# Performance work log

Measured on AMD Instinct MI355X. Metric: run time of the kernel, lower is better.

The kernel has to match this reference:

```python
import jax, jax.numpy as jnp
import numpy as np

N = 8            # n_qubits
N_LAYERS_CRZ = 1

_H = jnp.array([[1.0, 1.0], [1.0, -1.0]], dtype=jnp.complex64) / np.sqrt(2).astype(np.float32)
_X2 = jnp.array([[0.0, 1.0], [1.0, 0.0]], dtype=jnp.complex64)
_I2 = jnp.eye(2, dtype=jnp.complex64)


def _apply_1q(state, U, q):
    # shared (2,2) gate on wire q; state: (B, 2,...,2)
    moved = jnp.moveaxis(state, 1 + q, -1)
    out = jnp.einsum('ij,...j->...i', U, moved)
    return jnp.moveaxis(out, -1, 1 + q)


def _apply_1q_batched(state, U, q):
    # per-sample (B,2,2) gate on wire q
    moved = jnp.moveaxis(state, 1 + q, -1)
    out = jnp.einsum('bij,b...j->b...i', U, moved)
    return jnp.moveaxis(out, -1, 1 + q)


def _apply_diag_batched(state, d, q):
    # per-sample diagonal (B,2) phases on wire q
    shape = (d.shape[0],) + (1,) * q + (2,) + (1,) * (N - 1 - q)
    return state * d.reshape(shape)


def _apply_ctrl_diag(state, ph, c, t):
    # controlled diagonal: apply phases ph (2,) on target t when control c == 1
    moved = jnp.moveaxis(state, (1 + c, 1 + t), (-2, -1))
    d = jnp.stack([jnp.ones(2, state.dtype), ph])  # (bc, bt)
    moved = moved * d
    return jnp.moveaxis(moved, (-2, -1), (1 + c, 1 + t))


def _apply_ctrl(state, U, c, t):
    # controlled (2,2) gate, control c, target t
    moved = jnp.moveaxis(state, (1 + c, 1 + t), (-2, -1))
    s0 = moved[..., 0, :]
    s1 = jnp.einsum('ij,...j->...i', U, moved[..., 1, :])
    out = jnp.stack([s0, s1], axis=-2)
    return jnp.moveaxis(out, (-2, -1), (1 + c, 1 + t))


def _circuit(X, weights):
    B = X.shape[0]
    state = jnp.zeros((B,) + (2,) * N, jnp.complex64)
    state = state.at[(slice(None),) + (0,) * N].set(1.0)

    # encoding: H, RZ(x[2q]), RY(x[2q+1]) on each wire q (2q+1 < 16 always)
    for q in range(N):
        state = _apply_1q(state, _H, q)
        th_z = X[:, 2 * q]
        d = jnp.stack([jnp.exp(-0.5j * th_z), jnp.exp(0.5j * th_z)], axis=-1)  # (B,2)
        state = _apply_diag_batched(state, d, q)
        half = 0.5 * X[:, 2 * q + 1]
        c, s = jnp.cos(half), jnp.sin(half)
        Ury = jnp.stack([jnp.stack([c, -s], -1), jnp.stack([s, c], -1)], -2)  # (B,2,2) real
        state = _apply_1q_batched(state, Ury, q)

    # CRZ ring
    for l in range(N_LAYERS_CRZ):
        for i in range(N):
            th = weights[l, i]
            ph = jnp.stack([jnp.exp(-0.5j * th), jnp.exp(0.5j * th)])
            state = _apply_ctrl_diag(state, ph, i, (i + 1) % N)

    # all-to-all CRX
    for i in range(N):
        for j in range(N):
            if j == i:
                continue
            half = 0.5 * weights[N_LAYERS_CRZ + i, j]
            Urx = jnp.cos(half) * _I2 + (-1j * jnp.sin(half)) * _X2
            state = _apply_ctrl(state, Urx, i, j)

    probs = jnp.real(state * jnp.conj(state)).reshape(B, 2 ** N)
    q_idx = jnp.arange(N)
    bits = (jnp.arange(2 ** N)[None, :] >> (N - 1 - q_idx)[:, None]) & 1  # (N, 2^N)
    signs = (1.0 - 2.0 * bits).astype(probs.dtype)
    return probs @ signs.T  # (B, N) <Z_q> expectations


def setup_inputs() -> dict:
    key = jax.random.key(0)
    k1, k2 = jax.random.split(key)
    X = jax.random.normal(k1, (16384, 2 * N), dtype=jnp.float32)
    weights = jax.random.normal(k2, (N_LAYERS_CRZ + N, (N_LAYERS_CRZ + N) * N), dtype=jnp.float32)
    return {"X": X, "weights": weights}


def reference(X, weights):
    return _circuit(X, weights)
```

## Files before the change

kernel.cpp:

```cpp
#include <hip/hip_runtime.h>


static __device__ __forceinline__ float rlane(float v, int src) {
    return __int_as_float(__builtin_amdgcn_readlane(__float_as_int(v), src));
}
template <int CTRL>
static __device__ __forceinline__ float dppf(float x) {
    return __int_as_float(__builtin_amdgcn_update_dpp(0, __float_as_int(x), CTRL, 0xF, 0xF, true));
}
static __device__ __forceinline__ float xor1f(float x) { return dppf<0xB1>(x); }
static __device__ __forceinline__ float xor2f(float x) { return dppf<0x4E>(x); }
static __device__ __forceinline__ float xor4f(float x) { return dppf<0x1B>(dppf<0x141>(x)); }
static __device__ __forceinline__ float xor8f(float x) { return dppf<0x128>(x); }
static __device__ __forceinline__ float xorMf(float x, int m) {
    if (m == 1) return xor1f(x);
    if (m == 2) return xor2f(x);
    if (m == 4) return xor4f(x);
    return xor8f(x);
}
static __device__ __forceinline__ float2 xorM2(float2 a, int m) {
    float2 t; t.x = xorMf(a.x, m); t.y = xorMf(a.y, m); return t;
}
static __device__ __forceinline__ float2 cmul(float2 a, float2 b) {
    float2 t;
    t.x = a.x * b.x - a.y * b.y;
    t.y = a.x * b.y + a.y * b.x;
    return t;
}
static __device__ __forceinline__ float2 rotA(float2 t, float2 u, float c, float s) {
    float2 d;
    d.x = c * t.x + s * u.y;
    d.y = c * t.y - s * u.x;
    return d;
}

__global__ __launch_bounds__(256, 4) void qsim_kernel(const float* __restrict__ X,
                                                      const float* __restrict__ W,
                                                      float* __restrict__ out,
                                                      int B) {
    const int lane = threadIdx.x & 63;
    const int g = lane >> 4;
    const int s = lane & 15;
    const int b = (blockIdx.x * 4 + (threadIdx.x >> 6)) * 4 + g;
    const bool active = (b < B);
    const int bc = active ? b : (B - 1);

    float gcv = 1.0f, gsv = 0.0f;
    if (lane < 56) {
        const int i = lane / 7;
        const int jj = lane - 7 * i;
        const int j = jj + (jj >= i ? 1 : 0);
        const float h = 0.5f * W[(1 + i) * 72 + j];
        __sincosf(h, &gsv, &gcv);
    }

    float u0r, u0i, u1r, u1i;
    {
        const int q = s & 7;
        float2 xq = ((const float2*)X)[bc * 8 + q];
        float cz, sz, cy, sy;
        __sincosf(0.5f * xq.x, &sz, &cz);
        __sincosf(0.5f * xq.y, &sy, &cy);
        u0r = (cy - sy) * cz;  u0i = -(cy + sy) * sz;
        u1r = (cy + sy) * cz;  u1i = (cy - sy) * sz;
    }

    float2 P; P.x = 1.0f; P.y = 0.0f;
#pragma unroll
    for (int q = 4; q < 8; ++q) {
        const int src = (g << 4) + q;
        const float a0r = __shfl(u0r, src, 64), a0i = __shfl(u0i, src, 64);
        const float a1r = __shfl(u1r, src, 64), a1i = __shfl(u1i, src, 64);
        const int bit = (s >> (7 - q)) & 1;
        float2 v; v.x = bit ? a1r : a0r; v.y = bit ? a1i : a0i;
        P = cmul(P, v);
    }
    float2 w0[4], w1[4];
#pragma unroll
    for (int k = 0; k < 4; ++k) {
        const int src = (g << 4) + k;
        w0[k].x = __shfl(u0r, src, 64);  w0[k].y = __shfl(u0i, src, 64);
        w1[k].x = __shfl(u1r, src, 64);  w1[k].y = __shfl(u1i, src, 64);
    }
    float2 a[16];
    {
        float2 t1[2];
        t1[0] = w0[0];
        t1[1] = w1[0];
        float2 t2[4];
#pragma unroll
        for (int h = 0; h < 2; ++h) {
            t2[h * 2 + 0] = cmul(t1[h], w0[1]);
            t2[h * 2 + 1] = cmul(t1[h], w1[1]);
        }
        float2 t3[8];
#pragma unroll
        for (int h = 0; h < 4; ++h) {
            t3[h * 2 + 0] = cmul(t2[h], w0[2]);
            t3[h * 2 + 1] = cmul(t2[h], w1[2]);
        }
#pragma unroll
        for (int h = 0; h < 8; ++h) {
            a[h * 2 + 0] = cmul(P, cmul(t3[h], w0[3]));
            a[h * 2 + 1] = cmul(P, cmul(t3[h], w1[3]));
        }
    }

    {
        const float wv0 = W[0], wv1 = W[1], wv2 = W[2], wv3 = W[3];
        const float wv4 = W[4], wv5 = W[5], wv6 = W[6], wv7 = W[7];
        const int s3 = (s >> 3) & 1, s2 = (s >> 2) & 1, s1 = (s >> 1) & 1, s0 = s & 1;
        float phiS = 0.0f;
        phiS += s3 ? (s2 ? wv4 : -wv4) : 0.0f;
        phiS += s2 ? (s1 ? wv5 : -wv5) : 0.0f;
        phiS += s1 ? (s0 ? wv6 : -wv6) : 0.0f;
        const float termA = s3 ? wv3 : -wv3;
        const float termB = s0 ? wv7 : 0.0f;
#pragma unroll
        for (int r = 0; r < 16; ++r) {
            const int b3 = (r >> 3) & 1, b2 = (r >> 2) & 1, b1 = (r >> 1) & 1, b0 = r & 1;
            float phi = phiS + (b3 ? termB : -termB);
            if (b3) phi += b2 ? wv0 : -wv0;
            if (b2) phi += b1 ? wv1 : -wv1;
            if (b1) phi += b0 ? wv2 : -wv2;
            if (b0) phi += termA;
            float2 ph;
            __sincosf(0.5f * phi, &ph.y, &ph.x);
            a[r] = cmul(a[r], ph);
        }
    }

#pragma unroll
    for (int i = 0; i < 4; ++i) {
        float cg[8], sg[8];
#pragma unroll
        for (int j = 0; j < 8; ++j) {
            if (j == i) continue;
            const int gi = i * 7 + (j < i ? j : j - 1);
            cg[j] = rlane(gcv, gi);
            sg[j] = rlane(gsv, gi);
        }
        const int rc = 3 - i;
#pragma unroll
        for (int j = 0; j < 8; ++j) {
            if (j == i) continue;
            if (j < 4) {
                const int mt = 1 << (3 - j);
#pragma unroll
                for (int r = 0; r < 16; ++r) {
                    if (!((r >> rc) & 1)) continue;
                    if (r & mt) continue;
                    const int rp = r | mt;
                    const float2 t = a[r], u = a[rp];
                    a[r]  = rotA(t, u, cg[j], sg[j]);
                    a[rp] = rotA(u, t, cg[j], sg[j]);
                }
            } else {
                const int ms = 1 << (7 - j);
#pragma unroll
                for (int r = 0; r < 16; ++r) {
                    if (!((r >> rc) & 1)) continue;
                    const float2 p = xorM2(a[r], ms);
                    a[r] = rotA(a[r], p, cg[j], sg[j]);
                }
            }
        }
    }

#pragma unroll
    for (int k = 1; k <= 8; k <<= 1) {
        const bool sk = (s & k) != 0;
#pragma unroll
        for (int r = 0; r < 16; ++r) {
            if (r & k) continue;
            const int rp = r | k;
            const float2 tp = xorM2(a[rp], k);
            const float2 tr = xorM2(a[r],  k);
            a[r].x  = sk ? tp.x : a[r].x;
            a[r].y  = sk ? tp.y : a[r].y;
            a[rp].x = sk ? a[rp].x : tr.x;
            a[rp].y = sk ? a[rp].y : tr.y;
        }
    }

#pragma unroll
    for (int i = 4; i < 8; ++i) {
        float cg[8], sg[8];
#pragma unroll
        for (int j = 0; j < 8; ++j) {
            if (j == i) continue;
            const int gi = i * 7 + (j < i ? j : j - 1);
            cg[j] = rlane(gcv, gi);
            sg[j] = rlane(gsv, gi);
        }
        const int rc = 7 - i;
#pragma unroll
        for (int j = 0; j < 8; ++j) {
            if (j == i) continue;
            if (j < 4) {
                const int ms = 1 << (3 - j);
#pragma unroll
                for (int r = 0; r < 16; ++r) {
                    if (!((r >> rc) & 1)) continue;
                    const float2 p = xorM2(a[r], ms);
                    a[r] = rotA(a[r], p, cg[j], sg[j]);
                }
            } else {
                const int mt = 1 << (7 - j);
#pragma unroll
                for (int r = 0; r < 16; ++r) {
                    if (!((r >> rc) & 1)) continue;
                    if (r & mt) continue;
                    const int rp = r | mt;
                    const float2 t = a[r], u = a[rp];
                    a[r]  = rotA(t, u, cg[j], sg[j]);
                    a[rp] = rotA(u, t, cg[j], sg[j]);
                }
            }
        }
    }

    float p[16];
#pragma unroll
    for (int r = 0; r < 16; ++r) p[r] = a[r].x * a[r].x + a[r].y * a[r].y;
    float s8[8], E7 = 0.0f;
#pragma unroll
    for (int k = 0; k < 8; ++k) { s8[k] = p[2 * k] + p[2 * k + 1]; E7 += p[2 * k] - p[2 * k + 1]; }
    float s4[4], E6 = 0.0f;
#pragma unroll
    for (int k = 0; k < 4; ++k) { s4[k] = s8[2 * k] + s8[2 * k + 1]; E6 += s8[2 * k] - s8[2 * k + 1]; }
    float s2a[2], E5 = 0.0f;
#pragma unroll
    for (int k = 0; k < 2; ++k) { s2a[k] = s4[2 * k] + s4[2 * k + 1]; E5 += s4[2 * k] - s4[2 * k + 1]; }
    float A  = s2a[0] + s2a[1];
    float E4 = s2a[0] - s2a[1];
    float D0, D1, D2, D3;
    { const float t = xor1f(A); D0 = A - t; A += t;
      E4 += xor1f(E4); E5 += xor1f(E5); E6 += xor1f(E6); E7 += xor1f(E7); }
    { const float t = xor2f(A); D1 = A - t; A += t;
      D0 += xor2f(D0);
      E4 += xor2f(E4); E5 += xor2f(E5); E6 += xor2f(E6); E7 += xor2f(E7); }
    { const float t = xor4f(A); D2 = A - t; A += t;
      D0 += xor4f(D0); D1 += xor4f(D1);
      E4 += xor4f(E4); E5 += xor4f(E5); E6 += xor4f(E6); E7 += xor4f(E7); }
    { const float t = xor8f(A); D3 = A - t;
      D0 += xor8f(D0); D1 += xor8f(D1); D2 += xor8f(D2);
      E4 += xor8f(E4); E5 += xor8f(E5); E6 += xor8f(E6); E7 += xor8f(E7); }

    if (s == 0 && active) {
        const float sc = 1.0f / 256.0f;
        float* o = out + b * 8;
        o[0] = D3 * sc;
        o[1] = D2 * sc;
        o[2] = D1 * sc;
        o[3] = D0 * sc;
        o[4] = E4 * sc;
        o[5] = E5 * sc;
        o[6] = E6 * sc;
        o[7] = E7 * sc;
    }
}

extern "C" void kernel_launch(void* const* d_in, const int* in_sizes, int n_in,
                              void* d_out, int out_size, void* d_ws, size_t ws_size,
                              hipStream_t stream) {
    const float* X = (const float*)d_in[0];
    const float* W = (const float*)d_in[1];
    float* out = (float*)d_out;
    const int B = in_sizes[0] / 16;
    const int blocks = (B + 15) / 16;
    qsim_kernel<<<blocks, 256, 0, stream>>>(X, W, out, B);
}
```

Measured before the change: 76.86 us.

## Spread each sample's state over 32 lanes with 8 amplitudes per lane

Changes the state distribution from 16 lanes × 16 amplitudes to 32 lanes × 8 amplitudes per sample, so each wave handles two samples instead of four. The mid-circuit transpose between qubit halves is removed: gates controlled by lane-resident qubits are applied uniformly with a per-lane select of cos/sin. Cross-lane exchanges use DPP plus a ds_swizzle for the xor-16 partner. The aim is to cut register pressure (launch bounds raised to 8 waves per SIMD) and drop the shuffle-heavy transpose, at the cost of more cross-lane traffic and redundant rotations on lanes where the control bit is zero.

```diff
diff --git a/kernel.cpp b/kernel.cpp
--- a/kernel.cpp
+++ b/kernel.cpp
@@ -8,15 +8,19 @@
 static __device__ __forceinline__ float dppf(float x) {
     return __int_as_float(__builtin_amdgcn_update_dpp(0, __float_as_int(x), CTRL, 0xF, 0xF, true));
 }
-static __device__ __forceinline__ float xor1f(float x) { return dppf<0xB1>(x); }
-static __device__ __forceinline__ float xor2f(float x) { return dppf<0x4E>(x); }
-static __device__ __forceinline__ float xor4f(float x) { return dppf<0x1B>(dppf<0x141>(x)); }
-static __device__ __forceinline__ float xor8f(float x) { return dppf<0x128>(x); }
+static __device__ __forceinline__ float xor1f(float x)  { return dppf<0xB1>(x); }
+static __device__ __forceinline__ float xor2f(float x)  { return dppf<0x4E>(x); }
+static __device__ __forceinline__ float xor4f(float x)  { return dppf<0x1B>(dppf<0x141>(x)); }
+static __device__ __forceinline__ float xor8f(float x)  { return dppf<0x128>(x); }
+static __device__ __forceinline__ float xor16f(float x) {
+    return __int_as_float(__builtin_amdgcn_ds_swizzle(__float_as_int(x), 0x401F));
+}
 static __device__ __forceinline__ float xorMf(float x, int m) {
-    if (m == 1) return xor1f(x);
-    if (m == 2) return xor2f(x);
-    if (m == 4) return xor4f(x);
-    return xor8f(x);
+    if (m == 1)  return xor1f(x);
+    if (m == 2)  return xor2f(x);
+    if (m == 4)  return xor4f(x);
+    if (m == 8)  return xor8f(x);
+    return xor16f(x);
 }
 static __device__ __forceinline__ float2 xorM2(float2 a, int m) {
     float2 t; t.x = xorMf(a.x, m); t.y = xorMf(a.y, m); return t;
@@ -34,14 +38,14 @@
     return d;
 }
 
-__global__ __launch_bounds__(256, 4) void qsim_kernel(const float* __restrict__ X,
+__global__ __launch_bounds__(256, 8) void qsim_kernel(const float* __restrict__ X,
                                                       const float* __restrict__ W,
                                                       float* __restrict__ out,
                                                       int B) {
     const int lane = threadIdx.x & 63;
-    const int g = lane >> 4;
-    const int s = lane & 15;
-    const int b = (blockIdx.x * 4 + (threadIdx.x >> 6)) * 4 + g;
+    const int e  = lane >> 5;
+    const int s5 = lane & 31;
+    const int b = (blockIdx.x * 4 + (threadIdx.x >> 6)) * 2 + e;
     const bool active = (b < B);
     const int bc = active ? b : (B - 1);
 
@@ -56,7 +60,7 @@
 
     float u0r, u0i, u1r, u1i;
     {
-        const int q = s & 7;
+        const int q = s5 & 7;
         float2 xq = ((const float2*)X)[bc * 8 + q];
         float cz, sz, cy, sy;
         __sincosf(0.5f * xq.x, &sz, &cz);
@@ -67,22 +71,22 @@
 
     float2 P; P.x = 1.0f; P.y = 0.0f;
 #pragma unroll
-    for (int q = 4; q < 8; ++q) {
-        const int src = (g << 4) + q;
+    for (int q = 0; q < 5; ++q) {
+        const int src = (e << 5) + q;
         const float a0r = __shfl(u0r, src, 64), a0i = __shfl(u0i, src, 64);
         const float a1r = __shfl(u1r, src, 64), a1i = __shfl(u1i, src, 64);
-        const int bit = (s >> (7 - q)) & 1;
+        const int bit = (s5 >> (4 - q)) & 1;
         float2 v; v.x = bit ? a1r : a0r; v.y = bit ? a1i : a0i;
         P = cmul(P, v);
     }
-    float2 w0[4], w1[4];
-#pragma unroll
-    for (int k = 0; k < 4; ++k) {
-        const int src = (g << 4) + k;
+    float2 w0[3], w1[3];
+#pragma unroll
+    for (int k = 0; k < 3; ++k) {
+        const int src = (e << 5) + 5 + k;
         w0[k].x = __shfl(u0r, src, 64);  w0[k].y = __shfl(u0i, src, 64);
         w1[k].x = __shfl(u1r, src, 64);  w1[k].y = __shfl(u1i, src, 64);
     }
-    float2 a[16];
+    float2 a[8];
     {
         float2 t1[2];
         t1[0] = w0[0];
@@ -93,37 +97,32 @@
             t2[h * 2 + 0] = cmul(t1[h], w0[1]);
             t2[h * 2 + 1] = cmul(t1[h], w1[1]);
         }
-        float2 t3[8];
 #pragma unroll
         for (int h = 0; h < 4; ++h) {
-            t3[h * 2 + 0] = cmul(t2[h], w0[2]);
-            t3[h * 2 + 1] = cmul(t2[h], w1[2]);
-        }
-#pragma unroll
-        for (int h = 0; h < 8; ++h) {
-            a[h * 2 + 0] = cmul(P, cmul(t3[h], w0[3]));
-            a[h * 2 + 1] = cmul(P, cmul(t3[h], w1[3]));
+            a[h * 2 + 0] = cmul(P, cmul(t2[h], w0[2]));
+            a[h * 2 + 1] = cmul(P, cmul(t2[h], w1[2]));
         }
     }
 
     {
         const float wv0 = W[0], wv1 = W[1], wv2 = W[2], wv3 = W[3];
         const float wv4 = W[4], wv5 = W[5], wv6 = W[6], wv7 = W[7];
-        const int s3 = (s >> 3) & 1, s2 = (s >> 2) & 1, s1 = (s >> 1) & 1, s0 = s & 1;
+        const int s4b = (s5 >> 4) & 1, s3b = (s5 >> 3) & 1, s2b = (s5 >> 2) & 1;
+        const int s1b = (s5 >> 1) & 1, s0b = s5 & 1;
         float phiS = 0.0f;
-        phiS += s3 ? (s2 ? wv4 : -wv4) : 0.0f;
-        phiS += s2 ? (s1 ? wv5 : -wv5) : 0.0f;
-        phiS += s1 ? (s0 ? wv6 : -wv6) : 0.0f;
-        const float termA = s3 ? wv3 : -wv3;
-        const float termB = s0 ? wv7 : 0.0f;
-#pragma unroll
-        for (int r = 0; r < 16; ++r) {
-            const int b3 = (r >> 3) & 1, b2 = (r >> 2) & 1, b1 = (r >> 1) & 1, b0 = r & 1;
-            float phi = phiS + (b3 ? termB : -termB);
-            if (b3) phi += b2 ? wv0 : -wv0;
-            if (b2) phi += b1 ? wv1 : -wv1;
-            if (b1) phi += b0 ? wv2 : -wv2;
-            if (b0) phi += termA;
+        phiS += s4b ? (s3b ? wv0 : -wv0) : 0.0f;
+        phiS += s3b ? (s2b ? wv1 : -wv1) : 0.0f;
+        phiS += s2b ? (s1b ? wv2 : -wv2) : 0.0f;
+        phiS += s1b ? (s0b ? wv3 : -wv3) : 0.0f;
+        const float termA = s0b ? wv4 : 0.0f;
+        const float termB = s4b ? wv7 : -wv7;
+#pragma unroll
+        for (int r = 0; r < 8; ++r) {
+            const int b2 = (r >> 2) & 1, b1 = (r >> 1) & 1, b0 = r & 1;
+            float phi = phiS + (b2 ? termA : -termA);
+            if (b2) phi += b1 ? wv5 : -wv5;
+            if (b1) phi += b0 ? wv6 : -wv6;
+            if (b0) phi += termB;
             float2 ph;
             __sincosf(0.5f * phi, &ph.y, &ph.x);
             a[r] = cmul(a[r], ph);
@@ -131,7 +130,7 @@
     }
 
 #pragma unroll
-    for (int i = 0; i < 4; ++i) {
+    for (int i = 0; i < 8; ++i) {
         float cg[8], sg[8];
 #pragma unroll
         for (int j = 0; j < 8; ++j) {
@@ -140,121 +139,96 @@
             cg[j] = rlane(gcv, gi);
             sg[j] = rlane(gsv, gi);
         }
-        const int rc = 3 - i;
-#pragma unroll
-        for (int j = 0; j < 8; ++j) {
-            if (j == i) continue;
-            if (j < 4) {
-                const int mt = 1 << (3 - j);
-#pragma unroll
-                for (int r = 0; r < 16; ++r) {
-                    if (!((r >> rc) & 1)) continue;
-                    if (r & mt) continue;
-                    const int rp = r | mt;
-                    const float2 t = a[r], u = a[rp];
-                    a[r]  = rotA(t, u, cg[j], sg[j]);
-                    a[rp] = rotA(u, t, cg[j], sg[j]);
-                }
-            } else {
-                const int ms = 1 << (7 - j);
-#pragma unroll
-                for (int r = 0; r < 16; ++r) {
-                    if (!((r >> rc) & 1)) continue;
-                    const float2 p = xorM2(a[r], ms);
-                    a[r] = rotA(a[r], p, cg[j], sg[j]);
+        if (i <= 4) {
+            const int cbit = (s5 >> (4 - i)) & 1;
+#pragma unroll
+            for (int j = 0; j < 8; ++j) {
+                if (j == i) continue;
+                const float ce = cbit ? cg[j] : 1.0f;
+                const float se = cbit ? sg[j] : 0.0f;
+                if (j <= 4) {
+                    const int ms = 1 << (4 - j);
+#pragma unroll
+                    for (int r = 0; r < 8; ++r) {
+                        const float2 p = xorM2(a[r], ms);
+                        a[r] = rotA(a[r], p, ce, se);
+                    }
+                } else {
+                    const int mt = 1 << (7 - j);
+#pragma unroll
+                    for (int r = 0; r < 8; ++r) {
+                        if (r & mt) continue;
+                        const int rp = r | mt;
+                        const float2 t = a[r], u = a[rp];
+                        a[r]  = rotA(t, u, ce, se);
+                        a[rp] = rotA(u, t, ce, se);
+                    }
                 }
             }
-        }
-    }
-
-#pragma unroll
-    for (int k = 1; k <= 8; k <<= 1) {
-        const bool sk = (s & k) != 0;
-#pragma unroll
-        for (int r = 0; r < 16; ++r) {
-            if (r & k) continue;
-            const int rp = r | k;
-            const float2 tp = xorM2(a[rp], k);
-            const float2 tr = xorM2(a[r],  k);
-            a[r].x  = sk ? tp.x : a[r].x;
-            a[r].y  = sk ? tp.y : a[r].y;
-            a[rp].x = sk ? a[rp].x : tr.x;
-            a[rp].y = sk ? a[rp].y : tr.y;
-        }
-    }
-
-#pragma unroll
-    for (int i = 4; i < 8; ++i) {
-        float cg[8], sg[8];
-#pragma unroll
-        for (int j = 0; j < 8; ++j) {
-            if (j == i) continue;
-            const int gi = i * 7 + (j < i ? j : j - 1);
-            cg[j] = rlane(gcv, gi);
-            sg[j] = rlane(gsv, gi);
-        }
-        const int rc = 7 - i;
-#pragma unroll
-        for (int j = 0; j < 8; ++j) {
-            if (j == i) continue;
-            if (j < 4) {
-                const int ms = 1 << (3 - j);
-#pragma unroll
-                for (int r = 0; r < 16; ++r) {
-                    if (!((r >> rc) & 1)) continue;
-                    const float2 p = xorM2(a[r], ms);
-                    a[r] = rotA(a[r], p, cg[j], sg[j]);
-                }
-            } else {
-                const int mt = 1 << (7 - j);
-#pragma unroll
-                for (int r = 0; r < 16; ++r) {
-                    if (!((r >> rc) & 1)) continue;
-                    if (r & mt) continue;
-                    const int rp = r | mt;
-                    const float2 t = a[r], u = a[rp];
-                    a[r]  = rotA(t, u, cg[j], sg[j]);
-                    a[rp] = rotA(u, t, cg[j], sg[j]);
+        } else {
+            const int rc = 7 - i;
+#pragma unroll
+            for (int j = 0; j < 8; ++j) {
+                if (j == i) continue;
+                if (j <= 4) {
+                    const int ms = 1 << (4 - j);
+#pragma unroll
+                    for (int r = 0; r < 8; ++r) {
+                        if (!((r >> rc) & 1)) continue;
+                        const float2 p = xorM2(a[r], ms);
+                        a[r] = rotA(a[r], p, cg[j], sg[j]);
+                    }
+                } else {
+                    const int mt = 1 << (7 - j);
+#pragma unroll
+                    for (int r = 0; r < 8; ++r) {
+                        if (!((r >> rc) & 1)) continue;
+                        if (r & mt) continue;
+                        const int rp = r | mt;
+                        const float2 t = a[r], u = a[rp];
+                        a[r]  = rotA(t, u, cg[j], sg[j]);
+                        a[rp] = rotA(u, t, cg[j], sg[j]);
+                    }
                 }
             }
         }
     }
 
-    float p[16];
-#pragma unroll
-    for (int r = 0; r < 16; ++r) p[r] = a[r].x * a[r].x + a[r].y * a[r].y;
-    float s8[8], E7 = 0.0f;
-#pragma unroll
-    for (int k = 0; k < 8; ++k) { s8[k] = p[2 * k] + p[2 * k + 1]; E7 += p[2 * k] - p[2 * k + 1]; }
-    float s4[4], E6 = 0.0f;
-#pragma unroll
-    for (int k = 0; k < 4; ++k) { s4[k] = s8[2 * k] + s8[2 * k + 1]; E6 += s8[2 * k] - s8[2 * k + 1]; }
-    float s2a[2], E5 = 0.0f;
-#pragma unroll
-    for (int k = 0; k < 2; ++k) { s2a[k] = s4[2 * k] + s4[2 * k + 1]; E5 += s4[2 * k] - s4[2 * k + 1]; }
-    float A  = s2a[0] + s2a[1];
-    float E4 = s2a[0] - s2a[1];
-    float D0, D1, D2, D3;
-    { const float t = xor1f(A); D0 = A - t; A += t;
-      E4 += xor1f(E4); E5 += xor1f(E5); E6 += xor1f(E6); E7 += xor1f(E7); }
-    { const float t = xor2f(A); D1 = A - t; A += t;
+    float p[8];
+#pragma unroll
+    for (int r = 0; r < 8; ++r) p[r] = a[r].x * a[r].x + a[r].y * a[r].y;
+    float s4v[4], E7 = 0.0f;
+#pragma unroll
+    for (int k = 0; k < 4; ++k) { s4v[k] = p[2 * k] + p[2 * k + 1]; E7 += p[2 * k] - p[2 * k + 1]; }
+    float s2v[2], E6 = 0.0f;
+#pragma unroll
+    for (int k = 0; k < 2; ++k) { s2v[k] = s4v[2 * k] + s4v[2 * k + 1]; E6 += s4v[2 * k] - s4v[2 * k + 1]; }
+    float A  = s2v[0] + s2v[1];
+    float E5 = s2v[0] - s2v[1];
+    float D0, D1, D2, D3, D4;
+    { const float t = xor1f(A);  D0 = A - t; A += t;
+      E5 += xor1f(E5);  E6 += xor1f(E6);  E7 += xor1f(E7); }
+    { const float t = xor2f(A);  D1 = A - t; A += t;
       D0 += xor2f(D0);
-      E4 += xor2f(E4); E5 += xor2f(E5); E6 += xor2f(E6); E7 += xor2f(E7); }
-    { const float t = xor4f(A); D2 = A - t; A += t;
-      D0 += xor4f(D0); D1 += xor4f(D1);
-      E4 += xor4f(E4); E5 += xor4f(E5); E6 += xor4f(E6); E7 += xor4f(E7); }
-    { const float t = xor8f(A); D3 = A - t;
-      D0 += xor8f(D0); D1 += xor8f(D1); D2 += xor8f(D2);
-      E4 += xor8f(E4); E5 += xor8f(E5); E6 += xor8f(E6); E7 += xor8f(E7); }
-
-    if (s == 0 && active) {
+      E5 += xor2f(E5);  E6 += xor2f(E6);  E7 += xor2f(E7); }
+    { const float t = xor4f(A);  D2 = A - t; A += t;
+      D0 += xor4f(D0);  D1 += xor4f(D1);
+      E5 += xor4f(E5);  E6 += xor4f(E6);  E7 += xor4f(E7); }
+    { const float t = xor8f(A);  D3 = A - t; A += t;
+      D0 += xor8f(D0);  D1 += xor8f(D1);  D2 += xor8f(D2);
+      E5 += xor8f(E5);  E6 += xor8f(E6);  E7 += xor8f(E7); }
+    { const float t = xor16f(A); D4 = A - t;
+      D0 += xor16f(D0); D1 += xor16f(D1); D2 += xor16f(D2); D3 += xor16f(D3);
+      E5 += xor16f(E5); E6 += xor16f(E6); E7 += xor16f(E7); }
+
+    if (s5 == 0 && active) {
         const float sc = 1.0f / 256.0f;
         float* o = out + b * 8;
-        o[0] = D3 * sc;
-        o[1] = D2 * sc;
-        o[2] = D1 * sc;
-        o[3] = D0 * sc;
-        o[4] = E4 * sc;
+        o[0] = D4 * sc;
+        o[1] = D3 * sc;
+        o[2] = D2 * sc;
+        o[3] = D1 * sc;
+        o[4] = D0 * sc;
         o[5] = E5 * sc;
         o[6] = E6 * sc;
         o[7] = E7 * sc;
@@ -268,6 +242,6 @@
     const float* W = (const float*)d_in[1];
     float* out = (float*)d_out;
     const int B = in_sizes[0] / 16;
-    const int blocks = (B + 15) / 16;
+    const int blocks = (B + 7) / 8;
     qsim_kernel<<<blocks, 256, 0, stream>>>(X, W, out, B);
 }
```

After: 84.73 us. 10.3% more time.

## Roll CRX control loops with register bit-rotation to shrink code size

Applied to the files above, without the earlier changes.

The fully unrolled CRX loops over control qubits are replaced by non-unrolled loops (unroll 1). Each iteration always treats the upper half of the register array as the control=1 subset, then rotates the register bit indices so the next control qubit lands in the top bit. DPP cross-lane values are gathered into temporaries before the rotations are applied, which may improve instruction scheduling. The aim is smaller instruction footprint and lower register pressure, at the cost of loop overhead and register permutation moves that the compiler must resolve as copies.

```diff
diff --git a/kernel.cpp b/kernel.cpp
--- a/kernel.cpp
+++ b/kernel.cpp
@@ -17,9 +17,6 @@
     if (m == 2) return xor2f(x);
     if (m == 4) return xor4f(x);
     return xor8f(x);
-}
-static __device__ __forceinline__ float2 xorM2(float2 a, int m) {
-    float2 t; t.x = xorMf(a.x, m); t.y = xorMf(a.y, m); return t;
 }
 static __device__ __forceinline__ float2 cmul(float2 a, float2 b) {
     float2 t;
@@ -130,41 +127,44 @@
         }
     }
 
-#pragma unroll
-    for (int i = 0; i < 4; ++i) {
-        float cg[8], sg[8];
-#pragma unroll
-        for (int j = 0; j < 8; ++j) {
-            if (j == i) continue;
-            const int gi = i * 7 + (j < i ? j : j - 1);
-            cg[j] = rlane(gcv, gi);
-            sg[j] = rlane(gsv, gi);
-        }
-        const int rc = 3 - i;
-#pragma unroll
-        for (int j = 0; j < 8; ++j) {
-            if (j == i) continue;
-            if (j < 4) {
-                const int mt = 1 << (3 - j);
-#pragma unroll
-                for (int r = 0; r < 16; ++r) {
-                    if (!((r >> rc) & 1)) continue;
-                    if (r & mt) continue;
-                    const int rp = r | mt;
-                    const float2 t = a[r], u = a[rp];
-                    a[r]  = rotA(t, u, cg[j], sg[j]);
-                    a[rp] = rotA(u, t, cg[j], sg[j]);
-                }
-            } else {
-                const int ms = 1 << (7 - j);
-#pragma unroll
-                for (int r = 0; r < 16; ++r) {
-                    if (!((r >> rc) & 1)) continue;
-                    const float2 p = xorM2(a[r], ms);
-                    a[r] = rotA(a[r], p, cg[j], sg[j]);
-                }
-            }
-        }
+#pragma unroll 1
+    for (int it = 0; it < 4; ++it) {
+#pragma unroll
+        for (int tp = 2; tp >= 0; --tp) {
+            const int p = (tp - it) & 3;
+            const int j = 3 - p;
+            const int gi = it * 7 + (j < it ? j : j - 1);
+            const float c  = rlane(gcv, gi);
+            const float sn = rlane(gsv, gi);
+            const int mt = 1 << tp;
+#pragma unroll
+            for (int r = 8; r < 16; ++r) {
+                if (r & mt) continue;
+                const int rp = r | mt;
+                const float2 t = a[r], u = a[rp];
+                a[r]  = rotA(t, u, c, sn);
+                a[rp] = rotA(u, t, c, sn);
+            }
+        }
+#pragma unroll
+        for (int j = 4; j < 8; ++j) {
+            const int gi = it * 7 + (j - 1);
+            const float c  = rlane(gcv, gi);
+            const float sn = rlane(gsv, gi);
+            const int ms = 1 << (7 - j);
+            float pr[8], pi[8];
+#pragma unroll
+            for (int r = 8; r < 16; ++r) { pr[r - 8] = xorMf(a[r].x, ms); pi[r - 8] = xorMf(a[r].y, ms); }
+#pragma unroll
+            for (int r = 8; r < 16; ++r) {
+                float2 pp; pp.x = pr[r - 8]; pp.y = pi[r - 8];
+                a[r] = rotA(a[r], pp, c, sn);
+            }
+        }
+        { float2 t = a[8];  a[8]  = a[4];  a[4]  = a[2];  a[2]  = a[1];  a[1]  = t; }
+        { float2 t = a[9];  a[9]  = a[12]; a[12] = a[6];  a[6]  = a[3];  a[3]  = t; }
+        { float2 t = a[5];  a[5]  = a[10]; a[10] = t; }
+        { float2 t = a[11]; a[11] = a[13]; a[13] = a[14]; a[14] = a[7];  a[7]  = t; }
     }
 
 #pragma unroll
@@ -174,50 +174,55 @@
         for (int r = 0; r < 16; ++r) {
             if (r & k) continue;
             const int rp = r | k;
-            const float2 tp = xorM2(a[rp], k);
-            const float2 tr = xorM2(a[r],  k);
-            a[r].x  = sk ? tp.x : a[r].x;
-            a[r].y  = sk ? tp.y : a[r].y;
-            a[rp].x = sk ? a[rp].x : tr.x;
-            a[rp].y = sk ? a[rp].y : tr.y;
-        }
-    }
-
-#pragma unroll
-    for (int i = 4; i < 8; ++i) {
-        float cg[8], sg[8];
-#pragma unroll
-        for (int j = 0; j < 8; ++j) {
-            if (j == i) continue;
+            float2 tp2, tr2;
+            tp2.x = xorMf(a[rp].x, k); tp2.y = xorMf(a[rp].y, k);
+            tr2.x = xorMf(a[r].x,  k); tr2.y = xorMf(a[r].y,  k);
+            a[r].x  = sk ? tp2.x : a[r].x;
+            a[r].y  = sk ? tp2.y : a[r].y;
+            a[rp].x = sk ? a[rp].x : tr2.x;
+            a[rp].y = sk ? a[rp].y : tr2.y;
+        }
+    }
+
+#pragma unroll 1
+    for (int it = 0; it < 4; ++it) {
+        const int i = it + 4;
+#pragma unroll
+        for (int j = 0; j < 4; ++j) {
+            const int gi = i * 7 + j;
+            const float c  = rlane(gcv, gi);
+            const float sn = rlane(gsv, gi);
+            const int ms = 1 << (3 - j);
+            float pr[8], pi[8];
+#pragma unroll
+            for (int r = 8; r < 16; ++r) { pr[r - 8] = xorMf(a[r].x, ms); pi[r - 8] = xorMf(a[r].y, ms); }
+#pragma unroll
+            for (int r = 8; r < 16; ++r) {
+                float2 pp; pp.x = pr[r - 8]; pp.y = pi[r - 8];
+                a[r] = rotA(a[r], pp, c, sn);
+            }
+        }
+#pragma unroll
+        for (int tp = 2; tp >= 0; --tp) {
+            const int p = (tp - it) & 3;
+            const int j = 7 - p;
             const int gi = i * 7 + (j < i ? j : j - 1);
-            cg[j] = rlane(gcv, gi);
-            sg[j] = rlane(gsv, gi);
-        }
-        const int rc = 7 - i;
-#pragma unroll
-        for (int j = 0; j < 8; ++j) {
-            if (j == i) continue;
-            if (j < 4) {
-                const int ms = 1 << (3 - j);
-#pragma unroll
-                for (int r = 0; r < 16; ++r) {
-                    if (!((r >> rc) & 1)) continue;
-                    const float2 p = xorM2(a[r], ms);
-                    a[r] = rotA(a[r], p, cg[j], sg[j]);
-                }
-            } else {
-                const int mt = 1 << (7 - j);
-#pragma unroll
-                for (int r = 0; r < 16; ++r) {
-                    if (!((r >> rc) & 1)) continue;
-                    if (r & mt) continue;
-                    const int rp = r | mt;
-                    const float2 t = a[r], u = a[rp];
-                    a[r]  = rotA(t, u, cg[j], sg[j]);
-                    a[rp] = rotA(u, t, cg[j], sg[j]);
-                }
-            }
-        }
+            const float c  = rlane(gcv, gi);
+            const float sn = rlane(gsv, gi);
+            const int mt = 1 << tp;
+#pragma unroll
+            for (int r = 8; r < 16; ++r) {
+                if (r & mt) continue;
+                const int rp = r | mt;
+                const float2 t = a[r], u = a[rp];
+                a[r]  = rotA(t, u, c, sn);
+                a[rp] = rotA(u, t, c, sn);
+            }
+        }
+        { float2 t = a[8];  a[8]  = a[4];  a[4]  = a[2];  a[2]  = a[1];  a[1]  = t; }
+        { float2 t = a[9];  a[9]  = a[12]; a[12] = a[6];  a[6]  = a[3];  a[3]  = t; }
+        { float2 t = a[5];  a[5]  = a[10]; a[10] = t; }
+        { float2 t = a[11]; a[11] = a[13]; a[13] = a[14]; a[14] = a[7];  a[7]  = t; }
     }
 
     float p[16];
```

Measured after the change: 80.67 us. 1.05x slower.

## Precompute fixed entangling unitary and apply it via fp16 MFMA GEMM

Applied to the files above, without the earlier changes.

Splits the kernel in two. The first kernel builds the 256x256 unitary of the weight-only CRZ/CRX section by pushing basis vectors through the old gate code, and stores it as fp16 real and imaginary parts in the workspace. The second kernel builds each sample's product-state vector in LDS and multiplies it by that unitary with 16x16x32 f16 MFMA instructions, then reduces the probabilities to Z expectations. This replaces per-sample gate-by-gate simulation with a dense complex GEMM, at the cost of fp16 rounding error and an extra kernel launch.

```diff
diff --git a/kernel.cpp b/kernel.cpp
--- a/kernel.cpp
+++ b/kernel.cpp
@@ -1,5 +1,9 @@
 #include <hip/hip_runtime.h>
 
+
+typedef _Float16 half_t;
+typedef __attribute__((ext_vector_type(8))) _Float16 half8;
+typedef __attribute__((ext_vector_type(4))) float float4v;
 
 static __device__ __forceinline__ float rlane(float v, int src) {
     return __int_as_float(__builtin_amdgcn_readlane(__float_as_int(v), src));
@@ -34,16 +38,13 @@
     return d;
 }
 
-__global__ __launch_bounds__(256, 4) void qsim_kernel(const float* __restrict__ X,
-                                                      const float* __restrict__ W,
-                                                      float* __restrict__ out,
-                                                      int B) {
+__global__ __launch_bounds__(256, 4) void buildV_kernel(const float* __restrict__ W,
+                                                        half_t* __restrict__ Vr,
+                                                        half_t* __restrict__ Vi) {
     const int lane = threadIdx.x & 63;
     const int g = lane >> 4;
     const int s = lane & 15;
-    const int b = (blockIdx.x * 4 + (threadIdx.x >> 6)) * 4 + g;
-    const bool active = (b < B);
-    const int bc = active ? b : (B - 1);
+    const int eid = (blockIdx.x * 4 + (threadIdx.x >> 6)) * 4 + g;
 
     float gcv = 1.0f, gsv = 0.0f;
     if (lane < 56) {
@@ -54,56 +55,11 @@
         __sincosf(h, &gsv, &gcv);
     }
 
-    float u0r, u0i, u1r, u1i;
-    {
-        const int q = s & 7;
-        float2 xq = ((const float2*)X)[bc * 8 + q];
-        float cz, sz, cy, sy;
-        __sincosf(0.5f * xq.x, &sz, &cz);
-        __sincosf(0.5f * xq.y, &sy, &cy);
-        u0r = (cy - sy) * cz;  u0i = -(cy + sy) * sz;
-        u1r = (cy + sy) * cz;  u1i = (cy - sy) * sz;
-    }
-
-    float2 P; P.x = 1.0f; P.y = 0.0f;
-#pragma unroll
-    for (int q = 4; q < 8; ++q) {
-        const int src = (g << 4) + q;
-        const float a0r = __shfl(u0r, src, 64), a0i = __shfl(u0i, src, 64);
-        const float a1r = __shfl(u1r, src, 64), a1i = __shfl(u1i, src, 64);
-        const int bit = (s >> (7 - q)) & 1;
-        float2 v; v.x = bit ? a1r : a0r; v.y = bit ? a1i : a0i;
-        P = cmul(P, v);
-    }
-    float2 w0[4], w1[4];
-#pragma unroll
-    for (int k = 0; k < 4; ++k) {
-        const int src = (g << 4) + k;
-        w0[k].x = __shfl(u0r, src, 64);  w0[k].y = __shfl(u0i, src, 64);
-        w1[k].x = __shfl(u1r, src, 64);  w1[k].y = __shfl(u1i, src, 64);
-    }
     float2 a[16];
-    {
-        float2 t1[2];
-        t1[0] = w0[0];
-        t1[1] = w1[0];
-        float2 t2[4];
-#pragma unroll
-        for (int h = 0; h < 2; ++h) {
-            t2[h * 2 + 0] = cmul(t1[h], w0[1]);
-            t2[h * 2 + 1] = cmul(t1[h], w1[1]);
-        }
-        float2 t3[8];
-#pragma unroll
-        for (int h = 0; h < 4; ++h) {
-            t3[h * 2 + 0] = cmul(t2[h], w0[2]);
-            t3[h * 2 + 1] = cmul(t2[h], w1[2]);
-        }
-#pragma unroll
-        for (int h = 0; h < 8; ++h) {
-            a[h * 2 + 0] = cmul(P, cmul(t3[h], w0[3]));
-            a[h * 2 + 1] = cmul(P, cmul(t3[h], w1[3]));
-        }
+#pragma unroll
+    for (int r = 0; r < 16; ++r) {
+        a[r].x = (s == (eid & 15) && r == (eid >> 4)) ? 1.0f : 0.0f;
+        a[r].y = 0.0f;
     }
 
     {
@@ -220,44 +176,164 @@
         }
     }
 
-    float p[16];
-#pragma unroll
-    for (int r = 0; r < 16; ++r) p[r] = a[r].x * a[r].x + a[r].y * a[r].y;
-    float s8[8], E7 = 0.0f;
-#pragma unroll
-    for (int k = 0; k < 8; ++k) { s8[k] = p[2 * k] + p[2 * k + 1]; E7 += p[2 * k] - p[2 * k + 1]; }
-    float s4[4], E6 = 0.0f;
-#pragma unroll
-    for (int k = 0; k < 4; ++k) { s4[k] = s8[2 * k] + s8[2 * k + 1]; E6 += s8[2 * k] - s8[2 * k + 1]; }
-    float s2a[2], E5 = 0.0f;
-#pragma unroll
-    for (int k = 0; k < 2; ++k) { s2a[k] = s4[2 * k] + s4[2 * k + 1]; E5 += s4[2 * k] - s4[2 * k + 1]; }
-    float A  = s2a[0] + s2a[1];
-    float E4 = s2a[0] - s2a[1];
-    float D0, D1, D2, D3;
-    { const float t = xor1f(A); D0 = A - t; A += t;
-      E4 += xor1f(E4); E5 += xor1f(E5); E6 += xor1f(E6); E7 += xor1f(E7); }
-    { const float t = xor2f(A); D1 = A - t; A += t;
-      D0 += xor2f(D0);
-      E4 += xor2f(E4); E5 += xor2f(E5); E6 += xor2f(E6); E7 += xor2f(E7); }
-    { const float t = xor4f(A); D2 = A - t; A += t;
-      D0 += xor4f(D0); D1 += xor4f(D1);
-      E4 += xor4f(E4); E5 += xor4f(E5); E6 += xor4f(E6); E7 += xor4f(E7); }
-    { const float t = xor8f(A); D3 = A - t;
-      D0 += xor8f(D0); D1 += xor8f(D1); D2 += xor8f(D2);
-      E4 += xor8f(E4); E5 += xor8f(E5); E6 += xor8f(E6); E7 += xor8f(E7); }
-
-    if (s == 0 && active) {
-        const float sc = 1.0f / 256.0f;
-        float* o = out + b * 8;
-        o[0] = D3 * sc;
-        o[1] = D2 * sc;
-        o[2] = D1 * sc;
-        o[3] = D0 * sc;
-        o[4] = E4 * sc;
-        o[5] = E5 * sc;
-        o[6] = E6 * sc;
-        o[7] = E7 * sc;
+    const int ks = eid >> 5, kq = (eid >> 3) & 3, jj = eid & 7;
+#pragma unroll
+    for (int r = 0; r < 16; ++r) {
+        const int off = ((s * 8 + ks) * 64 + kq * 16 + r) * 8 + jj;
+        Vr[off] = (half_t)a[r].x;
+        Vi[off] = (half_t)a[r].y;
+    }
+}
+
+#define PSI_STRIDE 264
+
+__global__ __launch_bounds__(256, 2) void gemm_kernel(const float* __restrict__ X,
+                                                      const half_t* __restrict__ Vr,
+                                                      const half_t* __restrict__ Vi,
+                                                      float* __restrict__ out,
+                                                      int B) {
+    __shared__ float4 u_lds[32][8];
+    __shared__ half_t psir[32][PSI_STRIDE];
+    __shared__ half_t psii[32][PSI_STRIDE];
+    __shared__ float part[32][8][4];
+
+    const int tid = threadIdx.x;
+    const int rowbase = blockIdx.x * 32;
+
+    {
+        const int m = tid >> 3, q = tid & 7;
+        int row = rowbase + m; if (row >= B) row = B - 1;
+        const float2 xq = ((const float2*)X)[row * 8 + q];
+        float cz, sz, cy, sy;
+        __sincosf(0.5f * xq.x, &sz, &cz);
+        __sincosf(0.5f * xq.y, &sy, &cy);
+        float4 u;
+        u.x = (cy - sy) * cz;  u.y = -(cy + sy) * sz;
+        u.z = (cy + sy) * cz;  u.w = (cy - sy) * sz;
+        u_lds[m][q] = u;
+    }
+    __syncthreads();
+
+    {
+        const int m = tid >> 3, kh = tid & 7;
+        float2 uu[8][2];
+#pragma unroll
+        for (int q = 0; q < 8; ++q) {
+            const float4 u = u_lds[m][q];
+            uu[q][0].x = u.x; uu[q][0].y = u.y;
+            uu[q][1].x = u.z; uu[q][1].y = u.w;
+        }
+        const float2 pre = cmul(cmul(uu[0][(kh >> 2) & 1], uu[1][(kh >> 1) & 1]), uu[2][kh & 1]);
+        float2 t1[2], t2[4], t3[8], t4[16];
+        t1[0] = cmul(pre, uu[3][0]);  t1[1] = cmul(pre, uu[3][1]);
+#pragma unroll
+        for (int h = 0; h < 2; ++h) { t2[2*h] = cmul(t1[h], uu[4][0]); t2[2*h+1] = cmul(t1[h], uu[4][1]); }
+#pragma unroll
+        for (int h = 0; h < 4; ++h) { t3[2*h] = cmul(t2[h], uu[5][0]); t3[2*h+1] = cmul(t2[h], uu[5][1]); }
+#pragma unroll
+        for (int h = 0; h < 8; ++h) { t4[2*h] = cmul(t3[h], uu[6][0]); t4[2*h+1] = cmul(t3[h], uu[6][1]); }
+        unsigned int* pr = (unsigned int*)&psir[m][kh * 32];
+        unsigned int* pi = (unsigned int*)&psii[m][kh * 32];
+#pragma unroll
+        for (int h = 0; h < 16; ++h) {
+            const float2 v0 = cmul(t4[h], uu[7][0]);
+            const float2 v1 = cmul(t4[h], uu[7][1]);
+            union { half_t h2[2]; unsigned int u; } cr, ci;
+            cr.h2[0] = (half_t)v0.x; cr.h2[1] = (half_t)v1.x;
+            ci.h2[0] = (half_t)v0.y; ci.h2[1] = (half_t)v1.y;
+            pr[h] = cr.u; pi[h] = ci.u;
+        }
+    }
+    __syncthreads();
+
+    const int w = tid >> 6;
+    const int lane = tid & 63;
+    const int m16 = lane & 15;
+    float4v Cr[2][4], Ci[2][4];
+#pragma unroll
+    for (int rt = 0; rt < 2; ++rt)
+#pragma unroll
+        for (int t = 0; t < 4; ++t) {
+            Cr[rt][t] = (float4v){0.f, 0.f, 0.f, 0.f};
+            Ci[rt][t] = (float4v){0.f, 0.f, 0.f, 0.f};
+        }
+#pragma unroll
+    for (int ks = 0; ks < 8; ++ks) {
+        const int koff = ks * 32 + (lane >> 4) * 8;
+        const half8 Ar0 = *(const half8*)&psir[m16][koff];
+        const half8 Ai0 = *(const half8*)&psii[m16][koff];
+        const half8 Ar1 = *(const half8*)&psir[16 + m16][koff];
+        const half8 Ai1 = *(const half8*)&psii[16 + m16][koff];
+#pragma unroll
+        for (int t = 0; t < 4; ++t) {
+            const int T = w * 4 + t;
+            const int boff = ((T * 8 + ks) * 64 + lane) * 8;
+            const half8 Br = *(const half8*)(Vr + boff);
+            const half8 Bi = *(const half8*)(Vi + boff);
+            const half8 Bin = -Bi;
+            Cr[0][t] = __builtin_amdgcn_mfma_f32_16x16x32_f16(Ar0, Br,  Cr[0][t], 0, 0, 0);
+            Cr[0][t] = __builtin_amdgcn_mfma_f32_16x16x32_f16(Ai0, Bin, Cr[0][t], 0, 0, 0);
+            Ci[0][t] = __builtin_amdgcn_mfma_f32_16x16x32_f16(Ar0, Bi,  Ci[0][t], 0, 0, 0);
+            Ci[0][t] = __builtin_amdgcn_mfma_f32_16x16x32_f16(Ai0, Br,  Ci[0][t], 0, 0, 0);
+            Cr[1][t] = __builtin_amdgcn_mfma_f32_16x16x32_f16(Ar1, Br,  Cr[1][t], 0, 0, 0);
+            Cr[1][t] = __builtin_amdgcn_mfma_f32_16x16x32_f16(Ai1, Bin, Cr[1][t], 0, 0, 0);
+            Ci[1][t] = __builtin_amdgcn_mfma_f32_16x16x32_f16(Ar1, Bi,  Ci[1][t], 0, 0, 0);
+            Ci[1][t] = __builtin_amdgcn_mfma_f32_16x16x32_f16(Ai1, Br,  Ci[1][t], 0, 0, 0);
+        }
+    }
+
+    const float sw0 = ((w >> 1) & 1) ? -1.0f : 1.0f;
+    const float sw1 = (w & 1) ? -1.0f : 1.0f;
+    const int quad = lane >> 4;
+#pragma unroll
+    for (int rt = 0; rt < 2; ++rt) {
+        float A0[4] = {0.f, 0.f, 0.f, 0.f};
+        float A2[4] = {0.f, 0.f, 0.f, 0.f};
+        float A3[4] = {0.f, 0.f, 0.f, 0.f};
+#pragma unroll
+        for (int t = 0; t < 4; ++t) {
+            const int T = w * 4 + t;
+            const float s2 = ((T >> 1) & 1) ? -1.0f : 1.0f;
+            const float s3 = (T & 1) ? -1.0f : 1.0f;
+#pragma unroll
+            for (int reg = 0; reg < 4; ++reg) {
+                const float cr = Cr[rt][t][reg], ci = Ci[rt][t][reg];
+                const float P = cr * cr + ci * ci;
+                A0[reg] += P;
+                A2[reg] += s2 * P;
+                A3[reg] += s3 * P;
+            }
+        }
+#pragma unroll
+        for (int reg = 0; reg < 4; ++reg) {
+            float Z = A0[reg], E7, E6, E5, E4;
+            { const float tt = xor1f(Z); E7 = Z - tt; Z += tt; }
+            { const float tt = xor2f(Z); E6 = Z - tt; Z += tt; E7 += xor2f(E7); }
+            { const float tt = xor4f(Z); E5 = Z - tt; Z += tt; E7 += xor4f(E7); E6 += xor4f(E6); }
+            { const float tt = xor8f(Z); E4 = Z - tt; Z += tt; E7 += xor8f(E7); E6 += xor8f(E6); E5 += xor8f(E5); }
+            float Q2 = A2[reg]; Q2 += xor1f(Q2); Q2 += xor2f(Q2); Q2 += xor4f(Q2); Q2 += xor8f(Q2);
+            float Q3 = A3[reg]; Q3 += xor1f(Q3); Q3 += xor2f(Q3); Q3 += xor4f(Q3); Q3 += xor8f(Q3);
+            if (m16 == 0) {
+                const int m = rt * 16 + quad * 4 + reg;
+                part[m][0][w] = sw0 * Z;
+                part[m][1][w] = sw1 * Z;
+                part[m][2][w] = Q2;
+                part[m][3][w] = Q3;
+                part[m][4][w] = E4;
+                part[m][5][w] = E5;
+                part[m][6][w] = E6;
+                part[m][7][w] = E7;
+            }
+        }
+    }
+    __syncthreads();
+    {
+        const int m = tid >> 3, q = tid & 7;
+        const int row = rowbase + m;
+        if (row < B) {
+            const float v = part[m][q][0] + part[m][q][1] + part[m][q][2] + part[m][q][3];
+            out[row * 8 + q] = v * (1.0f / 256.0f);
+        }
     }
 }
 
@@ -268,6 +344,8 @@
     const float* W = (const float*)d_in[1];
     float* out = (float*)d_out;
     const int B = in_sizes[0] / 16;
-    const int blocks = (B + 15) / 16;
-    qsim_kernel<<<blocks, 256, 0, stream>>>(X, W, out, B);
-}
+    half_t* Vr = (half_t*)d_ws;
+    half_t* Vi = Vr + 256 * 256;
+    buildV_kernel<<<16, 256, 0, stream>>>(W, Vr, Vi);
+    gemm_kernel<<<(B + 31) / 32, 256, 0, stream>>>(X, Vr, Vi, out, B);
+}
```

Result: slower. 81.53 us (+6.1%).
